# Kernel optimization log

Hardware: AMD Instinct MI355X
Metric: run time of the kernel (lower is better)

Reference implementation:

```python
import jax, jax.numpy as jnp
import numpy as np

D_MODEL = 1024
N_HEADS = 16
HEAD_SIZE = D_MODEL // N_HEADS
D_FF = 4096
EPS = 1e-6


def _layernorm(x, g, b):
    # Faithful to source: (x + mean) / (std + eps), unbiased std (torch default)
    mean = jnp.mean(x, axis=-1, keepdims=True)
    std = jnp.std(x, axis=-1, keepdims=True, ddof=1)
    return g * ((x + mean) / (std + EPS)) + b


def setup_inputs() -> dict:
    key = jax.random.key(0)
    ks = jax.random.split(key, 12)
    s = lambda fan_in: 1.0 / np.sqrt(fan_in)
    x = jax.random.normal(ks[0], (4, 2048, D_MODEL), dtype=jnp.float32)
    Wq = jax.random.uniform(ks[1], (N_HEADS, D_MODEL, HEAD_SIZE), jnp.float32, -s(D_MODEL), s(D_MODEL))
    Wk = jax.random.uniform(ks[2], (N_HEADS, D_MODEL, HEAD_SIZE), jnp.float32, -s(D_MODEL), s(D_MODEL))
    Wv = jax.random.uniform(ks[3], (N_HEADS, D_MODEL, HEAD_SIZE), jnp.float32, -s(D_MODEL), s(D_MODEL))
    Wo = jax.random.uniform(ks[4], (D_MODEL, D_MODEL), jnp.float32, -s(D_MODEL), s(D_MODEL))
    bo = jax.random.uniform(ks[5], (D_MODEL,), jnp.float32, -s(D_MODEL), s(D_MODEL))
    W1 = jax.random.uniform(ks[6], (D_MODEL, D_FF), jnp.float32, -s(D_MODEL), s(D_MODEL))
    b1 = jax.random.uniform(ks[7], (D_FF,), jnp.float32, -s(D_MODEL), s(D_MODEL))
    W2 = jax.random.uniform(ks[8], (D_FF, D_MODEL), jnp.float32, -s(D_FF), s(D_FF))
    b2 = jax.random.uniform(ks[9], (D_MODEL,), jnp.float32, -s(D_FF), s(D_FF))
    g1 = jnp.ones((D_MODEL,), jnp.float32)
    be1 = jnp.zeros((D_MODEL,), jnp.float32)
    g2 = jnp.ones((D_MODEL,), jnp.float32)
    be2 = jnp.zeros((D_MODEL,), jnp.float32)
    return {"x": x, "Wq": Wq, "Wk": Wk, "Wv": Wv, "Wo": Wo, "bo": bo,
            "W1": W1, "b1": b1, "W2": W2, "b2": b2,
            "g1": g1, "be1": be1, "g2": g2, "be2": be2}


def reference(x, Wq, Wk, Wv, Wo, bo, W1, b1, W2, b2, g1, be1, g2, be2):
    # Multi-head attention; note: source scales by sqrt(d_model), not sqrt(head_size)
    scale = 1.0 / np.sqrt(D_MODEL)
    q = jnp.einsum('bsd,hde->bhse', x, Wq)
    k = jnp.einsum('bsd,hde->bhse', x, Wk)
    v = jnp.einsum('bsd,hde->bhse', x, Wv)
    scores = jnp.einsum('bhse,bhte->bhst', q, k) * scale
    attn = jax.nn.softmax(scores, axis=-1)
    o = jnp.einsum('bhst,bhte->bhse', attn, v)
    B, H, S, E = o.shape
    o = o.transpose(0, 2, 1, 3).reshape(B, S, H * E)  # concat heads
    mha_out = o @ Wo + bo

    h1 = _layernorm(x + mha_out, g1, be1)

    ff = jax.nn.relu(h1 @ W1 + b1) @ W2 + b2
    out = _layernorm(h1 + ff, g2, be2)
    return out
```

## Files before the change

kernel.cpp:

```cpp
#include <hip/hip_runtime.h>

typedef short short8 __attribute__((ext_vector_type(8)));
typedef short short4v __attribute__((ext_vector_type(4)));
typedef float floatx4 __attribute__((ext_vector_type(4)));

#define D_MODEL 1024
#define N_HEADS 16
#define HEAD    64
#define D_FF    4096
#define SEQ     2048
#define BATCH   4
#define TOKENS  (BATCH*SEQ)

__device__ __forceinline__ float b2f(unsigned short u) {
  return __uint_as_float(((unsigned)u) << 16);
}
__device__ __forceinline__ unsigned short f2b(float f) {
  unsigned u = __float_as_uint(f);
  unsigned r = 0x7fffu + ((u >> 16) & 1u);
  return (unsigned short)((u + r) >> 16);
}
__device__ __forceinline__ floatx4 mfma16(short8 a, short8 b, floatx4 c) {
  return __builtin_amdgcn_mfma_f32_16x16x32_bf16(a, b, c, 0, 0, 0);
}
__device__ __forceinline__ void load16_lds(const unsigned short* g, unsigned short* l) {
  __builtin_amdgcn_global_load_lds((const __attribute__((address_space(1))) void*)g,
                                   (__attribute__((address_space(3))) void*)l, 16, 0, 0);
}

__device__ __forceinline__ void transp_body(
    const float* __restrict__ src, unsigned short* __restrict__ dst,
    int R, int C, int bx, int by, float (*t)[65])
{
  int cb = bx * 64, rb = by * 64;
#pragma unroll
  for (int i = 0; i < 16; i++) {
    int idx = i * 256 + threadIdx.x;
    int lr = idx >> 6, lc = idx & 63;
    t[lr][lc] = src[(size_t)(rb + lr) * C + cb + lc];
  }
  __syncthreads();
#pragma unroll
  for (int i = 0; i < 16; i++) {
    int idx = i * 256 + threadIdx.x;
    int lc = idx >> 6, lr = idx & 63;
    dst[(size_t)(cb + lc) * R + rb + lr] = f2b(t[lr][lc]);
  }
}

__global__ __launch_bounds__(256) void prep_kernel(
    const float* __restrict__ x, unsigned short* __restrict__ x_bf,
    const float* __restrict__ Wq, const float* __restrict__ Wk,
    const float* __restrict__ Wv, unsigned short* __restrict__ qkv_bt,
    const float* __restrict__ Wo, unsigned short* __restrict__ wo_bt,
    const float* __restrict__ W1, unsigned short* __restrict__ w1_bt,
    const float* __restrict__ W2, unsigned short* __restrict__ w2_bt)
{
  __shared__ float t[64][65];
  int bid = blockIdx.x;
  if (bid < 8192) {
    int idx = bid * 1024 + threadIdx.x * 4;
    float4 v = *(const float4*)(x + idx);
    short4v o;
    o[0] = (short)f2b(v.x); o[1] = (short)f2b(v.y);
    o[2] = (short)f2b(v.z); o[3] = (short)f2b(v.w);
    *(short4v*)(x_bf + idx) = o;
  } else if (bid < 8960) {
    int by = bid - 8192;
    int xt = by & 15, z = by >> 4;
    int sel = z >> 4, h = z & 15;
    const float* W = (sel == 0) ? Wq : ((sel == 1) ? Wk : Wv);
    const float* src = W + (size_t)h * D_MODEL * HEAD;
    int rb = xt * 64;
#pragma unroll
    for (int i = 0; i < 16; i++) {
      int idx = i * 256 + threadIdx.x;
      int lr = idx >> 6, lc = idx & 63;
      t[lr][lc] = src[(size_t)(rb + lr) * HEAD + lc];
    }
    __syncthreads();
    unsigned short* d0 = qkv_bt + (size_t)(sel * 1024 + h * 64) * D_MODEL;
#pragma unroll
    for (int i = 0; i < 16; i++) {
      int idx = i * 256 + threadIdx.x;
      int lc = idx >> 6, lr = idx & 63;
      d0[(size_t)lc * D_MODEL + rb + lr] = f2b(t[lr][lc]);
    }
  } else if (bid < 9216) {
    int i = bid - 8960;
    transp_body(Wo, wo_bt, 1024, 1024, i & 15, i >> 4, t);
  } else if (bid < 10240) {
    int i = bid - 9216;
    transp_body(W1, w1_bt, 1024, 4096, i & 63, i >> 6, t);
  } else {
    int i = bid - 10240;
    transp_body(W2, w2_bt, 4096, 1024, i & 15, i >> 4, t);
  }
}

__global__ __launch_bounds__(512, 2) void gemm256(
    const unsigned short* __restrict__ A, const unsigned short* __restrict__ BT,
    const float* __restrict__ biasf, void* __restrict__ outp,
    int M, int N, int K, int epi)
{
  __shared__ unsigned short a_sh[2 * 256 * 64];
  __shared__ unsigned short b_sh[2 * 256 * 64];

  const int tid  = threadIdx.x;
  const int lane = tid & 63;
  const int wave = tid >> 6;
  const int quad = lane >> 4;
  const int l15  = lane & 15;
  const int wm   = wave >> 2;
  const int wn   = wave & 3;

  const int lin = blockIdx.y * gridDim.x + blockIdx.x;
  const int xcd = lin & 7, j = lin >> 3;
  const int m0 = (xcd * 4 + (j & 3)) * 256;
  const int n0 = (j >> 2) * 256;

  const int u  = tid >> 3;
  const int sc = (tid & 7) ^ (u & 7);
  const unsigned short* a_src = A  + (size_t)(m0 + u) * K + sc * 8;
  const int borig = ((u >> 5) * 64) + (u & 31);
  const unsigned short* b_src = BT + (size_t)(n0 + borig) * K + sc * 8;
  unsigned short* a_dst = a_sh + wave * 512;
  unsigned short* b_dst = b_sh + wave * 512;

#define SA(T, Rc)  load16_lds(a_src + (size_t)(Rc) * K + (T) * 64, \
                              a_dst + ((T) & 1) * 16384 + (Rc) * 64)
#define SB(T, Rb, Radd) load16_lds(b_src + (size_t)(Radd) * K + (T) * 64, \
                              b_dst + ((T) & 1) * 16384 + (Rb) * 64)
#define STG_A0(T) do { SA(T, 0);   SA(T, 128); } while (0)
#define STG_A1(T) do { SA(T, 64);  SA(T, 192); } while (0)
#define STG_B0(T) do { SB(T, 0, 0);    SB(T, 64, 128); } while (0)
#define STG_B1(T) do { SB(T, 128, 32); SB(T, 192, 160); } while (0)

  floatx4 acc[8][4] = {};
  short8 aF[4][2];
  short8 bF[2][2][2];
  const unsigned short* ash = a_sh;
  const unsigned short* bsh = b_sh;

#define LDA(QM) \
  _Pragma("unroll") for (int mi = 0; mi < 4; mi++) \
  _Pragma("unroll") for (int kh = 0; kh < 2; kh++) \
    aF[mi][kh] = *(const short8*)(ash + (wm * 128 + (QM) * 64 + mi * 16 + l15) * 64 \
                                  + (((kh * 4 + quad) ^ (l15 & 7)) * 8));
#define LDB(QN) \
  _Pragma("unroll") for (int ni = 0; ni < 2; ni++) \
  _Pragma("unroll") for (int kh = 0; kh < 2; kh++) \
    bF[QN][ni][kh] = *(const short8*)(bsh + ((QN) * 128 + wn * 32 + ni * 16 + l15) * 64 \
                                      + (((kh * 4 + quad) ^ (l15 & 7)) * 8));
#define MM(QM, QN) \
  _Pragma("unroll") for (int mi = 0; mi < 4; mi++) \
  _Pragma("unroll") for (int ni = 0; ni < 2; ni++) { \
    acc[(QM) * 4 + mi][(QN) * 2 + ni] = \
        mfma16(aF[mi][0], bF[QN][ni][0], acc[(QM) * 4 + mi][(QN) * 2 + ni]); \
    acc[(QM) * 4 + mi][(QN) * 2 + ni] = \
        mfma16(aF[mi][1], bF[QN][ni][1], acc[(QM) * 4 + mi][(QN) * 2 + ni]); \
  }
#define PH_VM(N) asm volatile("s_waitcnt vmcnt(" #N ")" ::: "memory");
#define PH_MID() \
  __builtin_amdgcn_s_barrier(); \
  asm volatile("s_waitcnt lgkmcnt(0)" ::: "memory"); \
  __builtin_amdgcn_sched_barrier(0); \
  __builtin_amdgcn_s_setprio(1);
#define PH_END() \
  __builtin_amdgcn_s_setprio(0); \
  __builtin_amdgcn_s_barrier();

  const int NT = K >> 6;

  STG_A0(0); STG_B0(0); STG_A1(0); STG_B1(0); STG_A0(1); STG_B0(1);
  PH_VM(4)
  __builtin_amdgcn_s_barrier();

  for (int t = 0; t < NT - 2; ++t) {
    ash = a_sh + (t & 1) * 16384;
    bsh = b_sh + (t & 1) * 16384;

    LDA(0) LDB(0)
    STG_A1(t + 1);
    PH_MID() MM(0, 0) PH_END();

    LDB(1)
    STG_B1(t + 1);
    PH_MID() MM(0, 1) PH_END();

    LDA(1)
    STG_A0(t + 2);
    PH_MID() MM(1, 0) PH_END();

    STG_B0(t + 2);
    PH_VM(4)
    PH_MID() MM(1, 1) PH_END();
  }
  {
    const int t = NT - 2;
    ash = a_sh + (t & 1) * 16384;
    bsh = b_sh + (t & 1) * 16384;

    LDA(0) LDB(0)
    STG_A1(t + 1);
    PH_MID() MM(0, 0) PH_END();

    LDB(1)
    STG_B1(t + 1);
    PH_MID() MM(0, 1) PH_END();

    LDA(1)
    PH_MID() MM(1, 0) PH_END();

    PH_VM(0)
    PH_MID() MM(1, 1) PH_END();
  }
  {
    const int t = NT - 1;
    ash = a_sh + (t & 1) * 16384;
    bsh = b_sh + (t & 1) * 16384;

    LDA(0) LDB(0)
    PH_MID() MM(0, 0) PH_END();

    LDB(1)
    PH_MID() MM(0, 1) PH_END();

    LDA(1)
    PH_MID() MM(1, 0) PH_END();

    PH_MID() MM(1, 1) PH_END();
  }

#undef SA
#undef SB
#undef STG_A0
#undef STG_A1
#undef STG_B0
#undef STG_B1
#undef LDA
#undef LDB
#undef MM
#undef PH_VM
#undef PH_MID
#undef PH_END

#pragma unroll
  for (int mi = 0; mi < 8; mi++) {
#pragma unroll
    for (int ni = 0; ni < 4; ni++) {
      const int col = n0 + wn * 64 + ni * 16 + l15;
      const int row0 = m0 + wm * 128 + mi * 16 + quad * 4;
      if (epi == 0) {
        int sel = col >> 10;
        int cc = col & 1023;
        int h = cc >> 6, e = cc & 63;
        int b = row0 >> 11, s0 = row0 & 2047;
        if (sel < 2) {
          unsigned short* base = (unsigned short*)outp + (size_t)sel * 8388608;
#pragma unroll
          for (int r = 0; r < 4; r++) {
            float v2 = (sel == 0) ? acc[mi][ni][r] * 0.04508422f : acc[mi][ni][r];
            base[((size_t)((b * N_HEADS + h) * SEQ + (s0 + r))) * HEAD + e] = f2b(v2);
          }
        } else {
          unsigned short* base = (unsigned short*)outp + (size_t)2 * 8388608;
          short4v pk;
#pragma unroll
          for (int r = 0; r < 4; r++) pk[r] = (short)f2b(acc[mi][ni][r]);
          *(short4v*)(base + ((size_t)((b * N_HEADS + h) * HEAD + e)) * SEQ + s0) = pk;
        }
      } else {
#pragma unroll
        for (int r = 0; r < 4; r++)
          ((unsigned short*)outp)[(size_t)(row0 + r) * N + col] =
              f2b(fmaxf(acc[mi][ni][r] + biasf[col], 0.0f));
      }
    }
  }
}

__global__ __launch_bounds__(512, 2) void gemm256n(
    const unsigned short* __restrict__ A, const unsigned short* __restrict__ BT,
    const float* __restrict__ biasf, const float* __restrict__ residf,
    const unsigned short* __restrict__ residb, void* __restrict__ outp,
    int M, int N, int K, int epi)
{
  __shared__ unsigned short a_sh[2 * 256 * 64];
  __shared__ unsigned short b_sh[2 * 128 * 64];

  const int tid  = threadIdx.x;
  const int lane = tid & 63;
  const int wave = tid >> 6;
  const int quad = lane >> 4;
  const int l15  = lane & 15;
  const int wm   = wave >> 1;
  const int wn   = wave & 1;

  const int lin = blockIdx.y * gridDim.x + blockIdx.x;
  const int xcd = lin & 7, j = lin >> 3;
  const int m0 = (xcd * 4 + (j & 3)) * 256;
  const int n0 = (j >> 2) * 128;

  const int u  = tid >> 3;
  const int sc = (tid & 7) ^ (u & 7);
  const unsigned short* a_src = A  + (size_t)(m0 + u) * K + sc * 8;
  const unsigned short* b_src = BT + (size_t)(n0 + u) * K + sc * 8;
  unsigned short* a_dst = a_sh + wave * 512;
  unsigned short* b_dst = b_sh + wave * 512;

#define SA(T, Rc) load16_lds(a_src + (size_t)(Rc) * K + (T) * 64, \
                             a_dst + ((T) & 1) * 16384 + (Rc) * 64)
#define SB(T, Rb) load16_lds(b_src + (size_t)(Rb) * K + (T) * 64, \
                             b_dst + ((T) & 1) * 8192 + (Rb) * 64)
#define STG_A0(T) do { SA(T, 0);   SA(T, 64);  } while (0)
#define STG_A1(T) do { SA(T, 128); SA(T, 192); } while (0)
#define STG_B(T)  do { SB(T, 0);   SB(T, 64);  } while (0)

  floatx4 acc[4][4] = {};
  short8 aF[2][2];
  short8 bF[2][2][2];
  const unsigned short* ash = a_sh;
  const unsigned short* bsh = b_sh;

#define LDA(QM) \
  _Pragma("unroll") for (int mi = 0; mi < 2; mi++) \
  _Pragma("unroll") for (int kh = 0; kh < 2; kh++) \
    aF[mi][kh] = *(const short8*)(ash + ((QM) * 128 + wm * 32 + mi * 16 + l15) * 64 \
                                  + (((kh * 4 + quad) ^ (l15 & 7)) * 8));
#define LDB(QN) \
  _Pragma("unroll") for (int ni = 0; ni < 2; ni++) \
  _Pragma("unroll") for (int kh = 0; kh < 2; kh++) \
    bF[QN][ni][kh] = *(const short8*)(bsh + ((QN) * 64 + wn * 32 + ni * 16 + l15) * 64 \
                                      + (((kh * 4 + quad) ^ (l15 & 7)) * 8));
#define MM2(QM) \
  _Pragma("unroll") for (int qn = 0; qn < 2; qn++) \
  _Pragma("unroll") for (int mi = 0; mi < 2; mi++) \
  _Pragma("unroll") for (int ni = 0; ni < 2; ni++) { \
    acc[(QM) * 2 + mi][qn * 2 + ni] = \
        mfma16(aF[mi][0], bF[qn][ni][0], acc[(QM) * 2 + mi][qn * 2 + ni]); \
    acc[(QM) * 2 + mi][qn * 2 + ni] = \
        mfma16(aF[mi][1], bF[qn][ni][1], acc[(QM) * 2 + mi][qn * 2 + ni]); \
  }
#define PH_VM(N) asm volatile("s_waitcnt vmcnt(" #N ")" ::: "memory");
#define PH_MID() \
  __builtin_amdgcn_s_barrier(); \
  asm volatile("s_waitcnt lgkmcnt(0)" ::: "memory"); \
  __builtin_amdgcn_sched_barrier(0); \
  __builtin_amdgcn_s_setprio(1);
#define PH_END() \
  __builtin_amdgcn_s_setprio(0); \
  __builtin_amdgcn_s_barrier();

  const int NT = K >> 6;

  STG_A0(0); STG_B(0); STG_A1(0); STG_A0(1); STG_B(1);
  PH_VM(4)
  __builtin_amdgcn_s_barrier();

  for (int t = 0; t < NT - 2; ++t) {
    ash = a_sh + (t & 1) * 16384;
    bsh = b_sh + (t & 1) * 8192;

    LDA(0) LDB(0) LDB(1)
    STG_A1(t + 1);
    PH_MID() MM2(0) PH_END();

    LDA(1)
    STG_A0(t + 2); STG_B(t + 2);
    PH_VM(4)
    PH_MID() MM2(1) PH_END();
  }
  {
    const int t = NT - 2;
    ash = a_sh + (t & 1) * 16384;
    bsh = b_sh + (t & 1) * 8192;

    LDA(0) LDB(0) LDB(1)
    STG_A1(t + 1);
    PH_MID() MM2(0) PH_END();

    LDA(1)
    PH_VM(0)
    PH_MID() MM2(1) PH_END();
  }
  {
    const int t = NT - 1;
    ash = a_sh + (t & 1) * 16384;
    bsh = b_sh + (t & 1) * 8192;

    LDA(0) LDB(0) LDB(1)
    PH_MID() MM2(0) PH_END();

    LDA(1)
    PH_MID() MM2(1) PH_END();
  }

#undef SA
#undef SB
#undef STG_A0
#undef STG_A1
#undef STG_B
#undef LDA
#undef LDB
#undef MM2
#undef PH_VM
#undef PH_MID
#undef PH_END

#pragma unroll
  for (int am = 0; am < 4; am++) {
    const int row0 = m0 + (am >> 1) * 128 + wm * 32 + (am & 1) * 16 + quad * 4;
#pragma unroll
    for (int bn = 0; bn < 4; bn++) {
      const int col = n0 + (bn >> 1) * 64 + wn * 32 + (bn & 1) * 16 + l15;
      if (epi == 1) {
#pragma unroll
        for (int r = 0; r < 4; r++)
          ((float*)outp)[(size_t)(row0 + r) * N + col] =
              acc[am][bn][r] + biasf[col] + residf[(size_t)(row0 + r) * N + col];
      } else {
#pragma unroll
        for (int r = 0; r < 4; r++)
          ((float*)outp)[(size_t)(row0 + r) * N + col] =
              acc[am][bn][r] + biasf[col] + b2f(residb[(size_t)(row0 + r) * N + col]);
      }
    }
  }
}

__global__ __launch_bounds__(256, 4) void attn_kernel(
    const unsigned short* __restrict__ q, const unsigned short* __restrict__ k,
    const unsigned short* __restrict__ vt, unsigned short* __restrict__ o)
{
  const int bh = blockIdx.y;
  const int qt = blockIdx.x;
  const int tid = threadIdx.x, lane = tid & 63, wave = tid >> 6;
  const int quad = lane >> 4, l15 = lane & 15;
  const size_t base = (size_t)bh * SEQ * HEAD;

  __shared__ unsigned short k_sh[64 * 64];
  __shared__ unsigned short vT_sh[64 * 64];
  __shared__ unsigned short p_sh[4 * 32 * 64];
  unsigned short* pw = p_sh + wave * 2048;

  short8 qf[2][2];
#pragma unroll
  for (int mj = 0; mj < 2; mj++) {
    const unsigned short* qp =
        q + base + (size_t)(qt * 128 + wave * 32 + mj * 16 + l15) * HEAD;
    qf[mj][0] = *(const short8*)(qp + quad * 8);
    qf[mj][1] = *(const short8*)(qp + 32 + quad * 8);
  }

  floatx4 oacc[2][4] = {};
  floatx4 rsacc[2] = {};

  short8 onesf;
  {
    short ov = (l15 == 0) ? (short)0x3F80 : (short)0;
#pragma unroll
    for (int jj = 0; jj < 8; jj++) onesf[jj] = ov;
  }

  const int r8 = lane >> 3, slot = lane & 7;

  for (int kt = 0; kt < SEQ / 64; kt++) {
    __syncthreads();
#pragma unroll
    for (int i = 0; i < 2; i++) {
      int t = wave * 16 + i * 8 + r8;
      int cg = slot ^ (t & 7);
      load16_lds(k + base + (size_t)(kt * 64 + t) * HEAD + cg * 8,
                 k_sh + (wave * 16 + i * 8) * 64);
      load16_lds(vt + base + (size_t)t * SEQ + kt * 64 + cg * 8,
                 vT_sh + (wave * 16 + i * 8) * 64);
    }
    __syncthreads();

#pragma unroll
    for (int ti = 0; ti < 4; ti++) {
      int t = ti * 16 + l15;
      short8 kf0 = *(const short8*)(k_sh + t * 64 + ((quad ^ (t & 7)) * 8));
      short8 kf1 = *(const short8*)(k_sh + t * 64 + (((4 + quad) ^ (t & 7)) * 8));
      floatx4 s0 = {0.f, 0.f, 0.f, 0.f}, s1 = {0.f, 0.f, 0.f, 0.f};
      __builtin_amdgcn_s_setprio(1);
      s0 = mfma16(kf0, qf[0][0], s0);
      s0 = mfma16(kf1, qf[0][1], s0);
      s1 = mfma16(kf0, qf[1][0], s1);
      s1 = mfma16(kf1, qf[1][1], s1);
      __builtin_amdgcn_s_setprio(0);
      const int pco = (((ti * 2 + (quad >> 1)) ^ (l15 & 7)) << 3) + (quad & 1) * 4;
#pragma unroll
      for (int mj = 0; mj < 2; mj++) {
        floatx4 s = mj ? s1 : s0;
        float p0 = __builtin_amdgcn_exp2f(s[0]);
        float p1 = __builtin_amdgcn_exp2f(s[1]);
        float p2 = __builtin_amdgcn_exp2f(s[2]);
        float p3 = __builtin_amdgcn_exp2f(s[3]);
        uint2 u;
        u.x = __builtin_amdgcn_perm(__float_as_uint(p1), __float_as_uint(p0), 0x07060302u);
        u.y = __builtin_amdgcn_perm(__float_as_uint(p3), __float_as_uint(p2), 0x07060302u);
        *(uint2*)(pw + (mj * 16 + l15) * 64 + pco) = u;
      }
    }

    {
      short8 pf[2][2];
#pragma unroll
      for (int mj = 0; mj < 2; mj++) {
        pf[mj][0] = *(const short8*)(pw + (mj * 16 + l15) * 64 +
                                     ((quad ^ (l15 & 7)) << 3));
        pf[mj][1] = *(const short8*)(pw + (mj * 16 + l15) * 64 +
                                     (((4 + quad) ^ (l15 & 7)) << 3));
      }
      __builtin_amdgcn_s_setprio(1);
#pragma unroll
      for (int ni = 0; ni < 4; ni++) {
        int e = ni * 16 + l15;
        short8 bv0 = *(const short8*)(vT_sh + e * 64 + ((quad ^ (e & 7)) * 8));
        short8 bv1 = *(const short8*)(vT_sh + e * 64 + (((4 + quad) ^ (e & 7)) * 8));
#pragma unroll
        for (int mj = 0; mj < 2; mj++) {
          oacc[mj][ni] = mfma16(pf[mj][0], bv0, oacc[mj][ni]);
          oacc[mj][ni] = mfma16(pf[mj][1], bv1, oacc[mj][ni]);
        }
      }
#pragma unroll
      for (int mj = 0; mj < 2; mj++) {
        rsacc[mj] = mfma16(pf[mj][0], onesf, rsacc[mj]);
        rsacc[mj] = mfma16(pf[mj][1], onesf, rsacc[mj]);
      }
      __builtin_amdgcn_s_setprio(0);
    }
  }

  const int b = bh >> 4, h = bh & 15;
#pragma unroll
  for (int mj = 0; mj < 2; mj++)
#pragma unroll
    for (int r = 0; r < 4; r++) {
      int s = qt * 128 + wave * 32 + mj * 16 + quad * 4 + r;
      float rsv = __shfl(rsacc[mj][r], quad * 16, 64);
      float inv = 1.0f / rsv;
#pragma unroll
      for (int ni = 0; ni < 4; ni++)
        o[((size_t)(b * SEQ + s)) * D_MODEL + h * HEAD + ni * 16 + l15] =
            f2b(oacc[mj][ni][r] * inv);
    }
}

__global__ __launch_bounds__(256) void ln_kernel(
    const float* __restrict__ in, const float* __restrict__ g,
    const float* __restrict__ be, void* __restrict__ outp, int write_bf16)
{
  const int row = blockIdx.x * 4 + (threadIdx.x >> 6);
  const int lane = threadIdx.x & 63;
  const float* xp = in + (size_t)row * D_MODEL;
  float4 xv[4];
  float s = 0.0f, ss = 0.0f;
#pragma unroll
  for (int j = 0; j < 4; j++) {
    xv[j] = *(const float4*)(xp + j * 256 + lane * 4);
    s += (xv[j].x + xv[j].y) + (xv[j].z + xv[j].w);
    ss += (xv[j].x * xv[j].x + xv[j].y * xv[j].y) +
          (xv[j].z * xv[j].z + xv[j].w * xv[j].w);
  }
#pragma unroll
  for (int m = 1; m < 64; m <<= 1) {
    s += __shfl_xor(s, m, 64);
    ss += __shfl_xor(ss, m, 64);
  }
  float mean = s * (1.0f / 1024.0f);
  float var = fmaxf((ss - 1024.0f * mean * mean) * (1.0f / 1023.0f), 0.0f);
  float inv = 1.0f / (sqrtf(var) + 1e-6f);
#pragma unroll
  for (int j = 0; j < 4; j++) {
    int c = j * 256 + lane * 4;
    float4 g4 = *(const float4*)(g + c);
    float4 b4 = *(const float4*)(be + c);
    float y0 = g4.x * ((xv[j].x + mean) * inv) + b4.x;
    float y1 = g4.y * ((xv[j].y + mean) * inv) + b4.y;
    float y2 = g4.z * ((xv[j].z + mean) * inv) + b4.z;
    float y3 = g4.w * ((xv[j].w + mean) * inv) + b4.w;
    if (write_bf16) {
      short4v o4;
      o4[0] = (short)f2b(y0); o4[1] = (short)f2b(y1);
      o4[2] = (short)f2b(y2); o4[3] = (short)f2b(y3);
      *(short4v*)((unsigned short*)outp + (size_t)row * D_MODEL + c) = o4;
    } else {
      float4 o4 = {y0, y1, y2, y3};
      *(float4*)((float*)outp + (size_t)row * D_MODEL + c) = o4;
    }
  }
}

extern "C" void kernel_launch(void* const* d_in, const int* in_sizes, int n_in,
                              void* d_out, int out_size, void* d_ws, size_t ws_size,
                              hipStream_t stream)
{
  const float* x   = (const float*)d_in[0];
  const float* Wq  = (const float*)d_in[1];
  const float* Wk  = (const float*)d_in[2];
  const float* Wv  = (const float*)d_in[3];
  const float* Wo  = (const float*)d_in[4];
  const float* bo  = (const float*)d_in[5];
  const float* W1  = (const float*)d_in[6];
  const float* b1  = (const float*)d_in[7];
  const float* W2  = (const float*)d_in[8];
  const float* b2  = (const float*)d_in[9];
  const float* g1  = (const float*)d_in[10];
  const float* be1 = (const float*)d_in[11];
  const float* g2  = (const float*)d_in[12];
  const float* be2 = (const float*)d_in[13];
  float* out = (float*)d_out;

  unsigned short* ws     = (unsigned short*)d_ws;
  unsigned short* w1_bt  = ws;
  unsigned short* w2_bt  = ws + 4194304;
  unsigned short* qkv_bt = ws + 8388608;
  unsigned short* wo_bt  = ws + 11534336;
  unsigned short* x_bf   = ws + 12582912;
  unsigned short* qws    = ws + 20971520;
  unsigned short* kws    = ws + 29360128;
  unsigned short* vws    = ws + 37748736;
  unsigned short* ows    = x_bf;
  float*          r1     = (float*)(ws + 20971520);
  unsigned short* h1_bf  = x_bf;
  unsigned short* ff1    = ws + 20971520;

  dim3 blk(256);

  prep_kernel<<<11264, blk, 0, stream>>>(x, x_bf, Wq, Wk, Wv, qkv_bt,
                                         Wo, wo_bt, W1, w1_bt, W2, w2_bt);

  gemm256<<<dim3(3072 / 256, TOKENS / 256), dim3(512), 0, stream>>>(
      x_bf, qkv_bt, nullptr, qws, TOKENS, 3072, 1024, 0);
  attn_kernel<<<dim3(SEQ / 128, BATCH * N_HEADS), blk, 0, stream>>>(qws, kws, vws, ows);
  gemm256n<<<dim3(1024 / 128, TOKENS / 256), dim3(512), 0, stream>>>(
      ows, wo_bt, bo, x, nullptr, r1, TOKENS, 1024, 1024, 1);
  ln_kernel<<<TOKENS / 4, blk, 0, stream>>>(r1, g1, be1, h1_bf, 1);
  gemm256<<<dim3(4096 / 256, TOKENS / 256), dim3(512), 0, stream>>>(
      h1_bf, w1_bt, b1, ff1, TOKENS, 4096, 1024, 2);
  gemm256n<<<dim3(1024 / 128, TOKENS / 256), dim3(512), 0, stream>>>(
      ff1, w2_bt, b2, nullptr, h1_bf, out, TOKENS, 1024, 4096, 3);
  ln_kernel<<<TOKENS / 4, blk, 0, stream>>>(out, g2, be2, out, 0);
}
```

Baseline: 474.2 us.

## Prefetch next K/V tile into registers while computing current attention tile

Replaces the direct global-to-LDS loads at the top of each key tile with register prefetching. Before computing on the current tile, the loop issues global loads for the next one, then writes them to LDS after compute, between two barriers. This hides global-load latency behind the MFMA and exp work. The cost is extra VGPRs for the staged data, which may reduce occupancy, and it drops the direct-to-LDS load path.

```diff
diff --git a/kernel.cpp b/kernel.cpp
--- a/kernel.cpp
+++ b/kernel.cpp
@@ -464,19 +464,34 @@
   }
 
   const int r8 = lane >> 3, slot = lane & 7;
+  const int t0 = wave * 16 + r8, t1 = wave * 16 + 8 + r8;
+  const int cg0 = slot ^ (t0 & 7), cg1 = slot ^ (t1 & 7);
+  const unsigned short* kg = k + base;
+  const unsigned short* vg = vt + base;
+  unsigned short* kd0 = k_sh + (size_t)t0 * 64 + slot * 8;
+  unsigned short* kd1 = k_sh + (size_t)t1 * 64 + slot * 8;
+  unsigned short* vd0 = vT_sh + (size_t)t0 * 64 + slot * 8;
+  unsigned short* vd1 = vT_sh + (size_t)t1 * 64 + slot * 8;
+
+  uint4 kr0, kr1, vr0, vr1;
+#define LOADREGS(KT) do { \
+    kr0 = *(const uint4*)(kg + (size_t)((KT) * 64 + t0) * HEAD + cg0 * 8); \
+    kr1 = *(const uint4*)(kg + (size_t)((KT) * 64 + t1) * HEAD + cg1 * 8); \
+    vr0 = *(const uint4*)(vg + (size_t)t0 * SEQ + (KT) * 64 + cg0 * 8);    \
+    vr1 = *(const uint4*)(vg + (size_t)t1 * SEQ + (KT) * 64 + cg1 * 8);    \
+  } while (0)
+#define DSWRITE() do { \
+    *(uint4*)kd0 = kr0; *(uint4*)kd1 = kr1; \
+    *(uint4*)vd0 = vr0; *(uint4*)vd1 = vr1; \
+  } while (0)
+
+  LOADREGS(0);
+  DSWRITE();
+  __syncthreads();
 
   for (int kt = 0; kt < SEQ / 64; kt++) {
-    __syncthreads();
-#pragma unroll
-    for (int i = 0; i < 2; i++) {
-      int t = wave * 16 + i * 8 + r8;
-      int cg = slot ^ (t & 7);
-      load16_lds(k + base + (size_t)(kt * 64 + t) * HEAD + cg * 8,
-                 k_sh + (wave * 16 + i * 8) * 64);
-      load16_lds(vt + base + (size_t)t * SEQ + kt * 64 + cg * 8,
-                 vT_sh + (wave * 16 + i * 8) * 64);
-    }
-    __syncthreads();
+    if (kt + 1 < SEQ / 64) LOADREGS(kt + 1);
+    __builtin_amdgcn_sched_barrier(0);
 
 #pragma unroll
     for (int ti = 0; ti < 4; ti++) {
@@ -533,7 +548,15 @@
       }
       __builtin_amdgcn_s_setprio(0);
     }
-  }
+
+    __syncthreads();
+    if (kt + 1 < SEQ / 64) {
+      DSWRITE();
+    }
+    __syncthreads();
+  }
+#undef LOADREGS
+#undef DSWRITE
 
   const int b = bh >> 4, h = bh & 15;
 #pragma unroll
```

New measurement: 467.7 us. No clear change (-1.4%).
